# Performance work log

Hardware: AMD Instinct MI355X
Metric: run time of the kernel (lower is better)

## Reference

```python
import jax, jax.numpy as jnp
import numpy as np

B, D, M, C = 256, 256, 65536, 1000
TEMP = 0.05
ALPHA_WEIGHT = 0.5
EPS = 1e-6


def setup_inputs() -> dict:
    key = jax.random.key(0)
    k = jax.random.split(key, 6)
    feat = jax.random.normal(k[0], (B, D), dtype=jnp.float32)
    features = jax.random.normal(k[1], (M, D), dtype=jnp.float32)
    features = features / jnp.clip(jnp.linalg.norm(features, axis=1, keepdims=True), 1e-12)
    sample_softlabels = jax.random.uniform(k[2], (M, C), dtype=jnp.float32)
    indexes = jax.random.randint(k[3], (B,), 0, M, dtype=jnp.int32)
    labels = jax.random.randint(k[4], (M,), 0, C, dtype=jnp.int32)
    batch_indexs_labels = jax.random.randint(k[5], (B,), 0, M, dtype=jnp.int32)
    return {
        "feat": feat,
        "features": features,
        "sample_softlabels": sample_softlabels,
        "indexes": indexes,
        "labels": labels,
        "batch_indexs_labels": batch_indexs_labels,
        "cur_epoch": 1,
    }


def reference(feat, features, sample_softlabels, indexes, labels, batch_indexs_labels, cur_epoch):
    # L2-normalize batch features (F.normalize with eps clamp)
    x = feat / jnp.clip(jnp.linalg.norm(feat, axis=1, keepdims=True), 1e-12)
    # HM.apply forward: similarity vs memory bank (memory momentum update is a
    # buffer side-effect and does not affect the returned loss)
    logits = (x @ features.T) / TEMP  # [B, M]
    # group similarities by class label of each memory slot (index_add_)
    sim = jax.ops.segment_sum(logits.T, labels, num_segments=C)  # [C, B]
    nums = jax.ops.segment_sum(jnp.ones((M,), jnp.float32), labels, num_segments=C)  # [C]
    mask = nums > 0
    sim = sim / jnp.where(mask, nums, 1.0)[:, None]  # class-mean similarity [C, B]
    simT = sim.T  # [B, C]
    # masked softmax over classes
    exps = jnp.exp(simT) * mask[None, :].astype(simT.dtype)
    probs = exps / (jnp.sum(exps, axis=1, keepdims=True) + EPS)
    log_probs = jnp.log(probs + EPS)  # [B, C]
    targets = labels[indexes]  # [B]
    loss1 = -jnp.mean(log_probs[jnp.arange(B), targets])
    if cur_epoch == 0:
        return loss1
    batch_soft_labels = sample_softlabels[batch_indexs_labels]  # [B, C]
    loss2 = jnp.sum(jnp.mean(-batch_soft_labels * log_probs, axis=0))
    return ALPHA_WEIGHT * loss1 + (1.0 - ALPHA_WEIGHT) * loss2
```

## Files before the change

### kernel.cpp

```cpp
#include <hip/hip_runtime.h>
#include <hip/hip_bf16.h>

#define B_SZ 256
#define D_SZ 256
#define M_SZ 65536
#define C_SZ 1000
#define TEMP 0.05f
#define EPSF 1e-6f

#define CPB 2
#define NBLK_CSUM (C_SZ / CPB)
#define LCAP 512


#define OFF_FCT   0
#define OFF_NUMS  512000
#define OFF_ACC   516000
#define OFF_LCNT  516008

static __device__ __forceinline__ unsigned short f2bf(float f) {
    __hip_bfloat16 h = __float2bfloat16(f);
    return *reinterpret_cast<unsigned short*>(&h);
}
static __device__ __forceinline__ float bf2f(unsigned short u) {
    return __uint_as_float((unsigned)u << 16);
}

__launch_bounds__(1024)
__global__ void k_csum(const float* __restrict__ features,
                       const int* __restrict__ labels,
                       unsigned short* __restrict__ fct, int* __restrict__ nums,
                       float* __restrict__ acc, int* __restrict__ lcnt) {
    __shared__ int list[CPB][LCAP];
    __shared__ int lcur[CPB];
    __shared__ float4 red[CPB][8][64];
    int t = threadIdx.x, b = blockIdx.x;
    int c0 = b * CPB;

    if (t < CPB) lcur[t] = 0;
    if (b == 0 && t == 0) { acc[0] = 0.f; acc[1] = 0.f; lcnt[0] = 0; }
    __syncthreads();

    const int4* L4 = (const int4*)labels;
    #pragma unroll
    for (int k = 0; k < M_SZ / 4 / 1024; ++k) {
        int idx = k * 1024 + t;
        int4 l4 = L4[idx];
        int m0 = idx * 4;
        unsigned d;
        d = (unsigned)(l4.x - c0); if (d < CPB) list[d][atomicAdd(&lcur[d], 1)] = m0 + 0;
        d = (unsigned)(l4.y - c0); if (d < CPB) list[d][atomicAdd(&lcur[d], 1)] = m0 + 1;
        d = (unsigned)(l4.z - c0); if (d < CPB) list[d][atomicAdd(&lcur[d], 1)] = m0 + 2;
        d = (unsigned)(l4.w - c0); if (d < CPB) list[d][atomicAdd(&lcur[d], 1)] = m0 + 3;
    }
    __syncthreads();

    int g = t >> 9;
    int tt = t & 511;
    int s = tt >> 6;
    int lane = tt & 63;
    int c = c0 + g;
    int n = lcur[g];
    const int* ml = list[g];
    float4 a = make_float4(0.f, 0.f, 0.f, 0.f);
    #pragma unroll 2
    for (int i = s; i < n; i += 8) {
        float4 v = *(const float4*)&features[(size_t)ml[i] * D_SZ + lane * 4];
        a.x += v.x; a.y += v.y; a.z += v.z; a.w += v.w;
    }
    red[g][s][lane] = a;
    __syncthreads();
    if (s == 0) {
        float4 z = make_float4(0.f, 0.f, 0.f, 0.f);
        #pragma unroll
        for (int q = 0; q < 8; ++q) {
            float4 r = red[g][q][lane];
            z.x += r.x; z.y += r.y; z.z += r.z; z.w += r.w;
        }
        float scale = 1.0f / (TEMP * (float)(n > 0 ? n : 1));
        ushort4 o;
        o.x = f2bf(z.x * scale); o.y = f2bf(z.y * scale);
        o.z = f2bf(z.z * scale); o.w = f2bf(z.w * scale);
        *(ushort4*)&fct[(size_t)lane * (C_SZ * 4) + c * 4] = o;
        if (lane == 0) nums[c] = n;
    }
}

__launch_bounds__(1024)
__global__ void k_loss(const float* __restrict__ feat,
                       const unsigned short* __restrict__ fct,
                       const int* __restrict__ nums,
                       const float* __restrict__ soft,
                       const int* __restrict__ indexes,
                       const int* __restrict__ labels,
                       const int* __restrict__ bil,
                       const int* __restrict__ cur_epoch,
                       float* __restrict__ acc, int* __restrict__ lcnt,
                       float* __restrict__ out) {
    __shared__ float xs0[D_SZ], xs1[D_SZ];
    __shared__ float wred[16], wred2[16];
    __shared__ float bc0, bc1;
    __shared__ int tgt0, tgt1, sr0, sr1;

    int t = threadIdx.x;
    int lane = t & 63, wid = t >> 6;
    int r0 = blockIdx.x * 2;

    if (t == 0) {
        tgt0 = labels[indexes[r0]];
        tgt1 = labels[indexes[r0 + 1]];
        sr0 = bil[r0];
        sr1 = bil[r0 + 1];
    }

    float v = (t < 512) ? feat[(size_t)r0 * D_SZ + t] : 0.f;
    float s = v * v;
    #pragma unroll
    for (int o = 32; o; o >>= 1) s += __shfl_down(s, o);
    if (lane == 0) wred[wid] = s;
    __syncthreads();
    if (t == 0) {
        bc0 = fmaxf(sqrtf(wred[0] + wred[1] + wred[2] + wred[3]), 1e-12f);
        bc1 = fmaxf(sqrtf(wred[4] + wred[5] + wred[6] + wred[7]), 1e-12f);
    }
    __syncthreads();
    if (t < 256) xs0[t] = v / bc0;
    else if (t < 512) xs1[t - 256] = v / bc1;
    __syncthreads();

    float a0 = 0.f, a1 = 0.f;
    if (t < C_SZ) {
        const ushort4* F = (const ushort4*)fct;
        #pragma unroll 4
        for (int j = 0; j < D_SZ / 4; ++j) {
            ushort4 u = F[(size_t)j * C_SZ + t];
            float4 x0 = *(const float4*)&xs0[4 * j];
            float4 x1 = *(const float4*)&xs1[4 * j];
            float fx = bf2f(u.x), fy = bf2f(u.y), fz = bf2f(u.z), fw = bf2f(u.w);
            a0 = fmaf(x0.x, fx, a0); a0 = fmaf(x0.y, fy, a0);
            a0 = fmaf(x0.z, fz, a0); a0 = fmaf(x0.w, fw, a0);
            a1 = fmaf(x1.x, fx, a1); a1 = fmaf(x1.y, fy, a1);
            a1 = fmaf(x1.z, fz, a1); a1 = fmaf(x1.w, fw, a1);
        }
    }
    float mk = (t < C_SZ && nums[t] > 0) ? 1.f : 0.f;
    float e0 = mk * __expf(a0);
    float e1 = mk * __expf(a1);

    float s0 = e0, s1 = e1;
    #pragma unroll
    for (int o = 32; o; o >>= 1) {
        s0 += __shfl_down(s0, o);
        s1 += __shfl_down(s1, o);
    }
    if (lane == 0) { wred[wid] = s0; wred2[wid] = s1; }
    __syncthreads();
    if (t == 0) {
        float z0 = 0.f, z1 = 0.f;
        #pragma unroll
        for (int i = 0; i < 16; ++i) { z0 += wred[i]; z1 += wred2[i]; }
        bc0 = z0; bc1 = z1;
    }
    __syncthreads();
    float inv0 = 1.0f / (bc0 + EPSF);
    float inv1 = 1.0f / (bc1 + EPSF);

    float p1 = 0.f, p2 = 0.f;
    if (t < C_SZ) {
        float lp0 = __logf(e0 * inv0 + EPSF);
        float lp1 = __logf(e1 * inv1 + EPSF);
        p2 = -(soft[(size_t)sr0 * C_SZ + t] * lp0 + soft[(size_t)sr1 * C_SZ + t] * lp1);
        if (t == tgt0) p1 -= lp0;
        if (t == tgt1) p1 -= lp1;
    }
    #pragma unroll
    for (int o = 32; o; o >>= 1) {
        p1 += __shfl_down(p1, o);
        p2 += __shfl_down(p2, o);
    }
    __syncthreads();
    if (lane == 0) { wred[wid] = p1; wred2[wid] = p2; }
    __syncthreads();
    if (t == 0) {
        float z1 = 0.f, z2 = 0.f;
        #pragma unroll
        for (int i = 0; i < 16; ++i) { z1 += wred[i]; z2 += wred2[i]; }
        atomicAdd(&acc[0], z1);
        atomicAdd(&acc[1], z2);
        __threadfence();
        int done = atomicAdd(lcnt, 1);
        if (done == (int)gridDim.x - 1) {
            float l1 = atomicAdd(&acc[0], 0.f) / (float)B_SZ;
            float l2 = atomicAdd(&acc[1], 0.f) / (float)B_SZ;
            out[0] = (cur_epoch[0] == 0) ? l1 : 0.5f * (l1 + l2);
        }
    }
}

extern "C" void kernel_launch(void* const* d_in, const int* in_sizes, int n_in,
                              void* d_out, int out_size, void* d_ws, size_t ws_size,
                              hipStream_t stream) {
    const float* feat     = (const float*)d_in[0];
    const float* features = (const float*)d_in[1];
    const float* soft     = (const float*)d_in[2];
    const int* indexes    = (const int*)d_in[3];
    const int* labels     = (const int*)d_in[4];
    const int* bil        = (const int*)d_in[5];
    const int* cur_epoch  = (const int*)d_in[6];

    char* ws = (char*)d_ws;
    unsigned short* fct = (unsigned short*)(ws + OFF_FCT);
    int* nums    = (int*)(ws + OFF_NUMS);
    float* acc   = (float*)(ws + OFF_ACC);
    int* lcnt    = (int*)(ws + OFF_LCNT);

    k_csum<<<NBLK_CSUM, 1024, 0, stream>>>(features, labels, fct, nums, acc, lcnt);
    k_loss<<<B_SZ / 2, 1024, 0, stream>>>(feat, fct, nums, soft, indexes, labels,
                                          bil, cur_epoch, acc, lcnt, (float*)d_out);
}
```

Before: 40.51 us.

## Split k_loss dot products over D quarters with 4 classes per thread

The loss kernel now has each thread compute four adjacent classes over one quarter of the feature dimension. It loads 16-byte vectors of bf16 class-mean features and reduces the partial sums through shared memory. After the reduction, only 250 threads do the exp/log/softmax work, and they read nums and the soft labels as vectors. This aims for wider, better-coalesced global loads and more independent FMA chains, at the cost of a shared-memory reduction, an extra barrier and more registers. Separately, the class-sum gather loop is unrolled further.

```diff
diff --git a/kernel.cpp b/kernel.cpp
--- a/kernel.cpp
+++ b/kernel.cpp
@@ -22,9 +22,8 @@
     __hip_bfloat16 h = __float2bfloat16(f);
     return *reinterpret_cast<unsigned short*>(&h);
 }
-static __device__ __forceinline__ float bf2f(unsigned short u) {
-    return __uint_as_float((unsigned)u << 16);
-}
+#define BFLO(u) __uint_as_float(((unsigned)(u)) << 16)
+#define BFHI(u) __uint_as_float(((unsigned)(u)) & 0xffff0000u)
 
 __launch_bounds__(1024)
 __global__ void k_csum(const float* __restrict__ features,
@@ -63,7 +62,7 @@
     int n = lcur[g];
     const int* ml = list[g];
     float4 a = make_float4(0.f, 0.f, 0.f, 0.f);
-    #pragma unroll 2
+    #pragma unroll 4
     for (int i = s; i < n; i += 8) {
         float4 v = *(const float4*)&features[(size_t)ml[i] * D_SZ + lane * 4];
         a.x += v.x; a.y += v.y; a.z += v.z; a.w += v.w;
@@ -98,6 +97,7 @@
                        float* __restrict__ acc, int* __restrict__ lcnt,
                        float* __restrict__ out) {
     __shared__ float xs0[D_SZ], xs1[D_SZ];
+    __shared__ float pa[4][256][9];
     __shared__ float wred[16], wred2[16];
     __shared__ float bc0, bc1;
     __shared__ int tgt0, tgt1, sr0, sr1;
@@ -128,26 +128,68 @@
     else if (t < 512) xs1[t - 256] = v / bc1;
     __syncthreads();
 
-    float a0 = 0.f, a1 = 0.f;
-    if (t < C_SZ) {
-        const ushort4* F = (const ushort4*)fct;
+    int q = t >> 8, tt = t & 255;
+    int c0 = 4 * tt;
+    float b00 = 0.f, b01 = 0.f, b02 = 0.f, b03 = 0.f;
+    float b10 = 0.f, b11 = 0.f, b12 = 0.f, b13 = 0.f;
+    if (tt < 250) {
+        int jb = q * 16;
         #pragma unroll 4
-        for (int j = 0; j < D_SZ / 4; ++j) {
-            ushort4 u = F[(size_t)j * C_SZ + t];
+        for (int j = jb; j < jb + 16; ++j) {
+            const unsigned short* base = fct + (size_t)j * (C_SZ * 4) + c0 * 4;
+            int4 u0 = *(const int4*)base;
+            int4 u1 = *(const int4*)(base + 8);
             float4 x0 = *(const float4*)&xs0[4 * j];
             float4 x1 = *(const float4*)&xs1[4 * j];
-            float fx = bf2f(u.x), fy = bf2f(u.y), fz = bf2f(u.z), fw = bf2f(u.w);
-            a0 = fmaf(x0.x, fx, a0); a0 = fmaf(x0.y, fy, a0);
-            a0 = fmaf(x0.z, fz, a0); a0 = fmaf(x0.w, fw, a0);
-            a1 = fmaf(x1.x, fx, a1); a1 = fmaf(x1.y, fy, a1);
-            a1 = fmaf(x1.z, fz, a1); a1 = fmaf(x1.w, fw, a1);
-        }
-    }
-    float mk = (t < C_SZ && nums[t] > 0) ? 1.f : 0.f;
-    float e0 = mk * __expf(a0);
-    float e1 = mk * __expf(a1);
-
-    float s0 = e0, s1 = e1;
+            float f0, f1, f2, f3;
+            f0 = BFLO(u0.x); f1 = BFHI(u0.x); f2 = BFLO(u0.y); f3 = BFHI(u0.y);
+            b00 = fmaf(x0.x, f0, b00); b00 = fmaf(x0.y, f1, b00);
+            b00 = fmaf(x0.z, f2, b00); b00 = fmaf(x0.w, f3, b00);
+            b10 = fmaf(x1.x, f0, b10); b10 = fmaf(x1.y, f1, b10);
+            b10 = fmaf(x1.z, f2, b10); b10 = fmaf(x1.w, f3, b10);
+            f0 = BFLO(u0.z); f1 = BFHI(u0.z); f2 = BFLO(u0.w); f3 = BFHI(u0.w);
+            b01 = fmaf(x0.x, f0, b01); b01 = fmaf(x0.y, f1, b01);
+            b01 = fmaf(x0.z, f2, b01); b01 = fmaf(x0.w, f3, b01);
+            b11 = fmaf(x1.x, f0, b11); b11 = fmaf(x1.y, f1, b11);
+            b11 = fmaf(x1.z, f2, b11); b11 = fmaf(x1.w, f3, b11);
+            f0 = BFLO(u1.x); f1 = BFHI(u1.x); f2 = BFLO(u1.y); f3 = BFHI(u1.y);
+            b02 = fmaf(x0.x, f0, b02); b02 = fmaf(x0.y, f1, b02);
+            b02 = fmaf(x0.z, f2, b02); b02 = fmaf(x0.w, f3, b02);
+            b12 = fmaf(x1.x, f0, b12); b12 = fmaf(x1.y, f1, b12);
+            b12 = fmaf(x1.z, f2, b12); b12 = fmaf(x1.w, f3, b12);
+            f0 = BFLO(u1.z); f1 = BFHI(u1.z); f2 = BFLO(u1.w); f3 = BFHI(u1.w);
+            b03 = fmaf(x0.x, f0, b03); b03 = fmaf(x0.y, f1, b03);
+            b03 = fmaf(x0.z, f2, b03); b03 = fmaf(x0.w, f3, b03);
+            b13 = fmaf(x1.x, f0, b13); b13 = fmaf(x1.y, f1, b13);
+            b13 = fmaf(x1.z, f2, b13); b13 = fmaf(x1.w, f3, b13);
+        }
+    }
+    pa[q][tt][0] = b00; pa[q][tt][1] = b10;
+    pa[q][tt][2] = b01; pa[q][tt][3] = b11;
+    pa[q][tt][4] = b02; pa[q][tt][5] = b12;
+    pa[q][tt][6] = b03; pa[q][tt][7] = b13;
+    __syncthreads();
+
+    float e0[4] = {0.f, 0.f, 0.f, 0.f};
+    float e1[4] = {0.f, 0.f, 0.f, 0.f};
+    float s0 = 0.f, s1 = 0.f;
+    if (t < 250) {
+        int4 nm = *(const int4*)&nums[4 * t];
+        #pragma unroll
+        for (int k = 0; k < 4; ++k) {
+            float a0 = (pa[0][t][2 * k] + pa[1][t][2 * k]) +
+                       (pa[2][t][2 * k] + pa[3][t][2 * k]);
+            float a1 = (pa[0][t][2 * k + 1] + pa[1][t][2 * k + 1]) +
+                       (pa[2][t][2 * k + 1] + pa[3][t][2 * k + 1]);
+            int nk = (k == 0) ? nm.x : (k == 1) ? nm.y : (k == 2) ? nm.z : nm.w;
+            float mk = (nk > 0) ? 1.f : 0.f;
+            e0[k] = mk * __expf(a0);
+            e1[k] = mk * __expf(a1);
+            s0 += e0[k];
+            s1 += e1[k];
+        }
+    }
+
     #pragma unroll
     for (int o = 32; o; o >>= 1) {
         s0 += __shfl_down(s0, o);
@@ -166,12 +208,20 @@
     float inv1 = 1.0f / (bc1 + EPSF);
 
     float p1 = 0.f, p2 = 0.f;
-    if (t < C_SZ) {
-        float lp0 = __logf(e0 * inv0 + EPSF);
-        float lp1 = __logf(e1 * inv1 + EPSF);
-        p2 = -(soft[(size_t)sr0 * C_SZ + t] * lp0 + soft[(size_t)sr1 * C_SZ + t] * lp1);
-        if (t == tgt0) p1 -= lp0;
-        if (t == tgt1) p1 -= lp1;
+    if (t < 250) {
+        int c0b = 4 * t;
+        float4 sp0 = *(const float4*)&soft[(size_t)sr0 * C_SZ + c0b];
+        float4 sp1 = *(const float4*)&soft[(size_t)sr1 * C_SZ + c0b];
+        #pragma unroll
+        for (int k = 0; k < 4; ++k) {
+            float w0 = (k == 0) ? sp0.x : (k == 1) ? sp0.y : (k == 2) ? sp0.z : sp0.w;
+            float w1 = (k == 0) ? sp1.x : (k == 1) ? sp1.y : (k == 2) ? sp1.z : sp1.w;
+            float lp0 = __logf(e0[k] * inv0 + EPSF);
+            float lp1 = __logf(e1[k] * inv1 + EPSF);
+            p2 -= w0 * lp0 + w1 * lp1;
+            if (c0b + k == tgt0) p1 -= lp0;
+            if (c0b + k == tgt1) p1 -= lp1;
+        }
     }
     #pragma unroll
     for (int o = 32; o; o >>= 1) {
```

Result: faster. 39.68 us (-2.0%).
